# Kernel tuning notes

Hardware: AMD Instinct MI355X
Metric: run time of the kernel (lower is better)

The kernel has to match this reference:

```python
import jax, jax.numpy as jnp
import numpy as np

B, T, D = 8, 1, 4096          # batch, fresh tokens (single-token decode), d_model
H, HD, KV = 32, 128, 512      # n_heads, head_dim, mla_kv_lrank
PAST = 8191                   # cached compressed-KV length
SCALE = HD ** -0.5


def setup_inputs() -> dict:
    key = jax.random.key(0)
    ks = jax.random.split(key, 6)
    return {
        "x": jax.random.normal(ks[0], (B, T, D), dtype=jnp.float32),
        "past_c": jax.random.normal(ks[1], (B, PAST, KV), dtype=jnp.float32),
        # absorbed q*k_up projection: [H, D, KV]
        "absorbed_qk": jax.random.normal(ks[2], (H, D, KV), dtype=jnp.float32) * 0.02,
        # _compress_kv: Linear(D -> KV)
        "w_compress": jax.random.normal(ks[3], (D, KV), dtype=jnp.float32) * 0.02,
        # v_up: Linear(KV -> H*HD)
        "w_v": jax.random.normal(ks[4], (KV, H * HD), dtype=jnp.float32) * 0.02,
        # out_proj: Linear(H*HD -> D)
        "w_o": jax.random.normal(ks[5], (H * HD, D), dtype=jnp.float32) * 0.02,
    }


def reference(x, past_c, absorbed_qk, w_compress, w_v, w_o):
    b, t, d = x.shape
    # compress fresh tokens and extend the compressed KV cache
    c = x @ w_compress                                 # [B, T, KV]
    c_full = jnp.concatenate([past_c, c], axis=1)      # [B, total, KV]
    total = c_full.shape[1]

    # absorbed query projection: Q_abs = x @ absorbed_qk per head
    q_abs = jnp.einsum('btd,hdk->bhtk', x, absorbed_qk)        # [B, H, T, KV]
    # attention scores directly against compressed cache
    scores = jnp.einsum('bhtk,bsk->bhts', q_abs, c_full) * SCALE  # [B, H, T, total]

    # causal mask: query t (absolute pos total-T+t) sees kv pos p iff p <= total-T+t
    q_pos = jnp.arange(t)[:, None] + (total - t)       # [T, 1]
    kv_pos = jnp.arange(total)[None, :]                # [1, total]
    causal = q_pos >= kv_pos                           # [T, total]
    scores = jnp.where(causal[None, None], scores, -jnp.inf)
    attn = jax.nn.softmax(scores, axis=-1)             # [B, H, T, total]

    # up-project V from compressed cache
    v = (c_full @ w_v).reshape(b, total, H, HD)        # [B, total, H, HD]
    out = jnp.einsum('bhts,bshd->bthd', attn, v).reshape(b, t, H * HD)
    return out @ w_o                                   # [B, T, D]
```

## Files before the change

kernel.cpp:

```cpp
#include <hip/hip_runtime.h>
#include <stdint.h>

#define B_ 8
#define D_ 4096
#define H_ 32
#define HD_ 128
#define KV_ 512
#define PAST_ 8191
#define SCALE_ 0.08838834764831845f

#define OFF_QABS 0u
#define OFF_CNEW 131072u
#define OFF_ML   135168u
#define OFF_CTXP 167936u
#define OFF_CTX  8556544u
#define OFF_CTX2 8687616u

typedef float f32x4 __attribute__((ext_vector_type(4)));
typedef float f32x2 __attribute__((ext_vector_type(2)));
typedef short s16x8 __attribute__((ext_vector_type(8)));
typedef short s16x4 __attribute__((ext_vector_type(4)));

__device__ __forceinline__ unsigned short f2bf(float f) {
    unsigned u = __float_as_uint(f);
    u = (u + 0x7FFFu + ((u >> 16) & 1u)) >> 16;
    return (unsigned short)u;
}
__device__ __forceinline__ float bf2f(unsigned short s) {
    return __uint_as_float(((unsigned)s) << 16);
}

__global__ __launch_bounds__(256) void k_qabs(const float* __restrict__ x,
                                              const float* __restrict__ aqk,
                                              const float* __restrict__ wc,
                                              float* __restrict__ ws) {
    const int h = blockIdx.x;
    const int dc = blockIdx.y;
    const int t = threadIdx.x;
    alignas(16) __shared__ float x_lds[B_][512];
    for (int i = t; i < B_ * 512; i += 256) {
        const int b = i >> 9, dd = i & 511;
        x_lds[b][dd] = x[b * D_ + dc * 512 + dd];
    }
    __syncthreads();
    const float* A = (h < H_) ? (aqk + (size_t)h * D_ * KV_) : wc;
    A += (size_t)(dc * 512) * KV_ + 2 * t;

    float acc[B_][2] = {};
    for (int dd = 0; dd < 512; dd += 4) {
        f32x2 a[4];
#pragma unroll
        for (int i = 0; i < 4; ++i)
            a[i] = *(const f32x2*)(A + (size_t)(dd + i) * KV_);
#pragma unroll
        for (int b = 0; b < B_; ++b) {
            const f32x4 xv = *(const f32x4*)&x_lds[b][dd];
            acc[b][0] += xv[0] * a[0][0] + xv[1] * a[1][0] + xv[2] * a[2][0] + xv[3] * a[3][0];
            acc[b][1] += xv[0] * a[0][1] + xv[1] * a[1][1] + xv[2] * a[2][1] + xv[3] * a[3][1];
        }
    }
#pragma unroll
    for (int b = 0; b < B_; ++b) {
        float* dst = (h < H_) ? (ws + OFF_QABS + (size_t)(b * H_ + h) * KV_ + 2 * t)
                              : (ws + OFF_CNEW + (size_t)b * KV_ + 2 * t);
        atomicAdd(dst, acc[b][0]);
        atomicAdd(dst + 1, acc[b][1]);
    }
}

__global__ __launch_bounds__(256, 2) void k_attn(const float* __restrict__ past_c,
                                                 float* __restrict__ ws) {
    const int bx = blockIdx.x;
    const int b = bx >> 6, sc = bx & 63;
    const int t = threadIdx.x;
    const int w = t >> 6, lane = t & 63, quad = lane >> 4, ln = lane & 15;
    const int ni = w & 1, kh = w >> 1;

    alignas(16) __shared__ unsigned short ch[16 * 520];
    alignas(16) __shared__ unsigned short cl[16 * 520];
    alignas(16) __shared__ unsigned short cT[512 * 20];
    alignas(16) __shared__ float Sp[2 * 16 * 33];
    alignas(16) __shared__ unsigned short P[32 * 20];
    __shared__ float alpha[32];

    s16x8 qh[8], ql[8];
    {
        const float* qp = ws + OFF_QABS + (size_t)(b * H_ + ni * 16 + ln) * KV_ + kh * 256 + quad * 8;
#pragma unroll
        for (int st = 0; st < 8; ++st) {
            const f32x4 v0 = *(const f32x4*)(qp + st * 32);
            const f32x4 v1 = *(const f32x4*)(qp + st * 32 + 4);
#pragma unroll
            for (int i = 0; i < 8; ++i) {
                const float xv = ((i < 4) ? v0[i] : v1[i - 4]) * SCALE_;
                const unsigned short hi = f2bf(xv);
                qh[st][i] = (short)hi;
                ql[st][i] = (short)f2bf(xv - bf2f(hi));
            }
        }
    }

    f32x4 cacc[16];
#pragma unroll
    for (int i = 0; i < 16; ++i) cacc[i] = (f32x4){0.f, 0.f, 0.f, 0.f};
    float m_run = -1e30f, l_run = 0.f;

    for (int sub = 0; sub < 8; ++sub) {
        const int s0 = sc * 128 + sub * 16;
        {
            const int r = t >> 4, cb = (t & 15) * 32;
            const int sg = s0 + r;
            const float* src = (sg == PAST_) ? (ws + OFF_CNEW + (size_t)b * KV_)
                                             : (past_c + ((size_t)b * PAST_ + sg) * KV_);
#pragma unroll
            for (int i = 0; i < 8; ++i) {
                const int k = cb + i * 4;
                const f32x4 v = *(const f32x4*)(src + k);
                s16x4 hi4, lo4;
#pragma unroll
                for (int e = 0; e < 4; ++e) {
                    const unsigned short hh = f2bf(v[e]);
                    hi4[e] = (short)hh;
                    lo4[e] = (short)f2bf(v[e] - bf2f(hh));
                    cT[(k + e) * 20 + r] = hh;
                }
                *(s16x4*)&ch[r * 520 + k] = hi4;
                *(s16x4*)&cl[r * 520 + k] = lo4;
            }
        }
        __syncthreads();
        {
            f32x4 sacc = {0.f, 0.f, 0.f, 0.f};
#pragma unroll
            for (int st = 0; st < 8; ++st) {
                const int ko = kh * 256 + st * 32 + quad * 8;
                const s16x8 ah = *(const s16x8*)&ch[ln * 520 + ko];
                const s16x8 al = *(const s16x8*)&cl[ln * 520 + ko];
                sacc = __builtin_amdgcn_mfma_f32_16x16x32_bf16(ah, qh[st], sacc, 0, 0, 0);
                sacc = __builtin_amdgcn_mfma_f32_16x16x32_bf16(ah, ql[st], sacc, 0, 0, 0);
                sacc = __builtin_amdgcn_mfma_f32_16x16x32_bf16(al, qh[st], sacc, 0, 0, 0);
            }
#pragma unroll
            for (int r = 0; r < 4; ++r)
                Sp[kh * 528 + (quad * 4 + r) * 33 + ni * 16 + ln] = sacc[r];
        }
        __syncthreads();
        if (t < 32) {
            const int h = t;
            float sv[16];
            float msub = -1e30f;
#pragma unroll
            for (int s = 0; s < 16; ++s) {
                sv[s] = Sp[s * 33 + h] + Sp[528 + s * 33 + h];
                msub = fmaxf(msub, sv[s]);
            }
            const float m_new = fmaxf(m_run, msub);
            const float al_ = __expf(m_run - m_new);
            float lsum = 0.f;
#pragma unroll
            for (int s = 0; s < 16; s += 2) {
                const float p0 = __expf(sv[s] - m_new);
                const float p1 = __expf(sv[s + 1] - m_new);
                lsum += p0 + p1;
                const unsigned pk = (unsigned)f2bf(p0) | ((unsigned)f2bf(p1) << 16);
                *(unsigned*)&P[h * 20 + s] = pk;
            }
            l_run = l_run * al_ + lsum;
            m_run = m_new;
            alpha[h] = al_;
        }
        __syncthreads();
        {
            const float av = alpha[ni * 16 + ln];
            const s16x4 bp = *(const s16x4*)&P[(ni * 16 + ln) * 20 + quad * 4];
#pragma unroll
            for (int ti = 0; ti < 16; ++ti) {
                const int krow = (kh * 16 + ti) * 16 + ln;
                const s16x4 ac = *(const s16x4*)&cT[krow * 20 + quad * 4];
                f32x4 cc = cacc[ti];
                cc[0] *= av; cc[1] *= av; cc[2] *= av; cc[3] *= av;
                cacc[ti] = __builtin_amdgcn_mfma_f32_16x16x16bf16_1k(ac, bp, cc, 0, 0, 0);
            }
        }
        __syncthreads();
    }
    {
        float* cp = ws + OFF_CTXP + ((size_t)(b * 64 + sc) * H_ + (ni * 16 + ln)) * KV_;
#pragma unroll
        for (int ti = 0; ti < 16; ++ti) {
            const int k0 = (kh * 16 + ti) * 16 + quad * 4;
            *(f32x4*)(cp + k0) = cacc[ti];
        }
    }
    if (t < 32) {
        float* mp = ws + OFF_ML + (size_t)(b * 64 + sc) * 64;
        mp[t] = m_run;
        mp[32 + t] = l_run;
    }
}

__global__ __launch_bounds__(256) void k_comb(float* __restrict__ ws) {
    const int b = blockIdx.x >> 5, h = blockIdx.x & 31;
    const int t = threadIdx.x;
    __shared__ float ml[64], ll[64];
    if (t < 64) {
        const float* mp = ws + OFF_ML + (size_t)(b * 64 + t) * 64;
        ml[t] = mp[h];
        ll[t] = mp[32 + h];
    }
    __syncthreads();
    float M = -1e30f;
    for (int sc = 0; sc < 64; ++sc) M = fmaxf(M, ml[sc]);
    float L = 0.f;
    for (int sc = 0; sc < 64; ++sc) L += ll[sc] * __expf(ml[sc] - M);
    const float invL = 1.f / L;
    float a0 = 0.f, a1 = 0.f;
    for (int sc = 0; sc < 64; ++sc) {
        const float wgt = __expf(ml[sc] - M) * invL;
        const float* cp = ws + OFF_CTXP + ((size_t)(b * 64 + sc) * H_ + h) * KV_;
        a0 += wgt * cp[t];
        a1 += wgt * cp[256 + t];
    }
    float* o = ws + OFF_CTX + (size_t)(b * H_ + h) * KV_;
    o[t] = a0;
    o[256 + t] = a1;
}

__global__ __launch_bounds__(256) void k_vup(const float* __restrict__ wv, float* __restrict__ ws) {
    const int b = blockIdx.x >> 5, h = blockIdx.x & 31;
    const int t = threadIdx.x;
    alignas(16) __shared__ float cx[512];
    __shared__ float red[256];
    cx[t] = ws[OFF_CTX + (size_t)(b * H_ + h) * KV_ + t];
    cx[t + 256] = ws[OFF_CTX + (size_t)(b * H_ + h) * KV_ + t + 256];
    __syncthreads();
    const int khalf = t >> 7, hd = t & 127;
    const float* wp = wv + (size_t)(khalf * 256) * (H_ * HD_) + h * HD_ + hd;
    float acc = 0.f;
#pragma unroll 8
    for (int k = 0; k < 256; ++k)
        acc += cx[khalf * 256 + k] * wp[(size_t)k * (H_ * HD_)];
    red[t] = acc;
    __syncthreads();
    if (t < 128)
        ws[OFF_CTX2 + (size_t)b * (H_ * HD_) + h * HD_ + t] = red[t] + red[128 + t];
}

__global__ __launch_bounds__(256) void k_out(const float* __restrict__ wo,
                                             const float* __restrict__ ws,
                                             float* __restrict__ out) {
    const int dc = blockIdx.x, jc = blockIdx.y;
    const int t = threadIdx.x;
    alignas(16) __shared__ float c2[B_][256];
#pragma unroll
    for (int i = 0; i < 8; ++i) {
        const int e = t + i * 256;
        const int bb = e >> 8, jj = e & 255;
        c2[bb][jj] = ws[OFF_CTX2 + (size_t)bb * D_ + jc * 256 + jj];
    }
    __syncthreads();
    const int d = dc * 256 + t;
    float acc[B_] = {};
    for (int j = 0; j < 256; j += 4) {
        const float w0 = wo[(size_t)(jc * 256 + j) * D_ + d];
        const float w1 = wo[(size_t)(jc * 256 + j + 1) * D_ + d];
        const float w2 = wo[(size_t)(jc * 256 + j + 2) * D_ + d];
        const float w3 = wo[(size_t)(jc * 256 + j + 3) * D_ + d];
#pragma unroll
        for (int b = 0; b < B_; ++b) {
            const f32x4 cv = *(const f32x4*)&c2[b][j];
            acc[b] += cv[0] * w0 + cv[1] * w1 + cv[2] * w2 + cv[3] * w3;
        }
    }
#pragma unroll
    for (int b = 0; b < B_; ++b)
        atomicAdd(&out[b * D_ + d], acc[b]);
}

extern "C" void kernel_launch(void* const* d_in, const int* in_sizes, int n_in,
                              void* d_out, int out_size, void* d_ws, size_t ws_size,
                              hipStream_t stream) {
    const float* x      = (const float*)d_in[0];
    const float* past_c = (const float*)d_in[1];
    const float* aqk    = (const float*)d_in[2];
    const float* wc     = (const float*)d_in[3];
    const float* wv     = (const float*)d_in[4];
    const float* wo     = (const float*)d_in[5];
    float* out = (float*)d_out;
    float* ws  = (float*)d_ws;

    hipMemsetAsync(ws, 0, (size_t)OFF_ML * sizeof(float), stream);
    hipMemsetAsync(d_out, 0, (size_t)out_size * sizeof(float), stream);

    k_qabs<<<dim3(33, 8), 256, 0, stream>>>(x, aqk, wc, ws);
    k_attn<<<dim3(512), 256, 0, stream>>>(past_c, ws);
    k_comb<<<dim3(256), 256, 0, stream>>>(ws);
    k_vup<<<dim3(256), 256, 0, stream>>>(wv, ws);
    k_out<<<dim3(16, 16), 256, 0, stream>>>(wo, ws, out);
}
```

Baseline: 595.0 us.

## Split q-abs reduction, swizzle cT LDS, fuse combine with V-up, widen loads

The q-abs projection now uses 16 D-chunks with 128 threads and float4 weight loads. It writes partial sums to the workspace, and a new reduction kernel adds them up, replacing float atomics and the workspace memset. In the attention kernel the transposed-cache LDS writes are XOR-swizzled to cut bank conflicts, and the global load pattern is changed. The softmax-combine and V-up kernels are fused into one with vectorized loads, which removes a launch and a workspace round trip. The output projection loop is unrolled by 8. The cost is an extra launch for the reduction and more workspace traffic for the partial sums.

```diff
diff --git a/kernel.cpp b/kernel.cpp
--- a/kernel.cpp
+++ b/kernel.cpp
@@ -9,12 +9,13 @@
 #define PAST_ 8191
 #define SCALE_ 0.08838834764831845f
 
-#define OFF_QABS 0u
-#define OFF_CNEW 131072u
-#define OFF_ML   135168u
-#define OFF_CTXP 167936u
-#define OFF_CTX  8556544u
-#define OFF_CTX2 8687616u
+#define OFF_QP   0u
+#define OFF_CP   2097152u
+#define OFF_QABS 2162688u
+#define OFF_CNEW 2293760u
+#define OFF_ML   2297856u
+#define OFF_CTXP 2330624u
+#define OFF_CTX2 10719232u
 
 typedef float f32x4 __attribute__((ext_vector_type(4)));
 typedef float f32x2 __attribute__((ext_vector_type(2)));
@@ -30,41 +31,69 @@
     return __uint_as_float(((unsigned)s) << 16);
 }
 
-__global__ __launch_bounds__(256) void k_qabs(const float* __restrict__ x,
+__global__ __launch_bounds__(128) void k_qabs(const float* __restrict__ x,
                                               const float* __restrict__ aqk,
                                               const float* __restrict__ wc,
                                               float* __restrict__ ws) {
     const int h = blockIdx.x;
     const int dc = blockIdx.y;
     const int t = threadIdx.x;
-    alignas(16) __shared__ float x_lds[B_][512];
-    for (int i = t; i < B_ * 512; i += 256) {
-        const int b = i >> 9, dd = i & 511;
-        x_lds[b][dd] = x[b * D_ + dc * 512 + dd];
+    alignas(16) __shared__ float x_lds[B_][256];
+    for (int i = t; i < 512; i += 128) {
+        const int b = i >> 6, g = i & 63;
+        *(f32x4*)&x_lds[b][g * 4] = *(const f32x4*)(x + (size_t)b * D_ + dc * 256 + g * 4);
     }
     __syncthreads();
     const float* A = (h < H_) ? (aqk + (size_t)h * D_ * KV_) : wc;
-    A += (size_t)(dc * 512) * KV_ + 2 * t;
-
-    float acc[B_][2] = {};
-    for (int dd = 0; dd < 512; dd += 4) {
-        f32x2 a[4];
-#pragma unroll
-        for (int i = 0; i < 4; ++i)
-            a[i] = *(const f32x2*)(A + (size_t)(dd + i) * KV_);
+    A += ((size_t)dc * 256) * KV_ + t * 4;
+
+    f32x4 acc[B_];
+#pragma unroll
+    for (int b = 0; b < B_; ++b) acc[b] = (f32x4){0.f, 0.f, 0.f, 0.f};
+
+#pragma unroll 2
+    for (int dd = 0; dd < 256; dd += 4) {
+        const f32x4 a0 = *(const f32x4*)(A + (size_t)(dd + 0) * KV_);
+        const f32x4 a1 = *(const f32x4*)(A + (size_t)(dd + 1) * KV_);
+        const f32x4 a2 = *(const f32x4*)(A + (size_t)(dd + 2) * KV_);
+        const f32x4 a3 = *(const f32x4*)(A + (size_t)(dd + 3) * KV_);
 #pragma unroll
         for (int b = 0; b < B_; ++b) {
-            const f32x4 xv = *(const f32x4*)&x_lds[b][dd];
-            acc[b][0] += xv[0] * a[0][0] + xv[1] * a[1][0] + xv[2] * a[2][0] + xv[3] * a[3][0];
-            acc[b][1] += xv[0] * a[0][1] + xv[1] * a[1][1] + xv[2] * a[2][1] + xv[3] * a[3][1];
+            const f32x4 xq = *(const f32x4*)&x_lds[b][dd];
+            acc[b] += xq.x * a0 + xq.y * a1 + xq.z * a2 + xq.w * a3;
         }
     }
 #pragma unroll
     for (int b = 0; b < B_; ++b) {
-        float* dst = (h < H_) ? (ws + OFF_QABS + (size_t)(b * H_ + h) * KV_ + 2 * t)
-                              : (ws + OFF_CNEW + (size_t)b * KV_ + 2 * t);
-        atomicAdd(dst, acc[b][0]);
-        atomicAdd(dst + 1, acc[b][1]);
+        float* dst = (h < H_)
+            ? (ws + OFF_QP + (size_t)dc * 131072u + (size_t)(b * H_ + h) * KV_ + t * 4)
+            : (ws + OFF_CP + (size_t)dc * 4096u + (size_t)b * KV_ + t * 4);
+        *(f32x4*)dst = acc[b];
+    }
+}
+
+__global__ __launch_bounds__(256) void k_qred(float* __restrict__ ws) {
+    const int bx = blockIdx.x;
+    const int t = threadIdx.x;
+    if (bx < 256) {
+        const int b = bx >> 5, h = bx & 31;
+        const size_t row = (size_t)(b * H_ + h) * KV_;
+        f32x2 s = {0.f, 0.f};
+#pragma unroll
+        for (int p = 0; p < 16; ++p) {
+            const f32x2 v = *(const f32x2*)(ws + OFF_QP + (size_t)p * 131072u + row + 2 * t);
+            s[0] += v[0]; s[1] += v[1];
+        }
+        *(f32x2*)(ws + OFF_QABS + row + 2 * t) = s;
+    } else {
+        const int b = bx - 256;
+        f32x2 s = {0.f, 0.f};
+#pragma unroll
+        for (int p = 0; p < 16; ++p) {
+            const f32x2 v = *(const f32x2*)(ws + OFF_CP + (size_t)p * 4096u + (size_t)b * KV_ + 2 * t);
+            s[0] += v[0]; s[1] += v[1];
+        }
+        *(f32x2*)(ws + OFF_CNEW + (size_t)b * KV_ + 2 * t) = s;
     }
 }
 
@@ -108,13 +137,13 @@
     for (int sub = 0; sub < 8; ++sub) {
         const int s0 = sc * 128 + sub * 16;
         {
-            const int r = t >> 4, cb = (t & 15) * 32;
+            const int r = t >> 4, m = t & 15;
             const int sg = s0 + r;
             const float* src = (sg == PAST_) ? (ws + OFF_CNEW + (size_t)b * KV_)
                                              : (past_c + ((size_t)b * PAST_ + sg) * KV_);
 #pragma unroll
             for (int i = 0; i < 8; ++i) {
-                const int k = cb + i * 4;
+                const int k = m * 4 + i * 64;
                 const f32x4 v = *(const f32x4*)(src + k);
                 s16x4 hi4, lo4;
 #pragma unroll
@@ -122,7 +151,8 @@
                     const unsigned short hh = f2bf(v[e]);
                     hi4[e] = (short)hh;
                     lo4[e] = (short)f2bf(v[e] - bf2f(hh));
-                    cT[(k + e) * 20 + r] = hh;
+                    const int kk = k + e;
+                    cT[kk * 20 + (r ^ ((((kk) >> 4) & 3) << 2))] = hh;
                 }
                 *(s16x4*)&ch[r * 520 + k] = hi4;
                 *(s16x4*)&cl[r * 520 + k] = lo4;
@@ -176,7 +206,8 @@
 #pragma unroll
             for (int ti = 0; ti < 16; ++ti) {
                 const int krow = (kh * 16 + ti) * 16 + ln;
-                const s16x4 ac = *(const s16x4*)&cT[krow * 20 + quad * 4];
+                const int sg2 = (quad ^ ((krow >> 4) & 3)) << 2;
+                const s16x4 ac = *(const s16x4*)&cT[krow * 20 + sg2];
                 f32x4 cc = cacc[ti];
                 cc[0] *= av; cc[1] *= av; cc[2] *= av; cc[3] *= av;
                 cacc[ti] = __builtin_amdgcn_mfma_f32_16x16x16bf16_1k(ac, bp, cc, 0, 0, 0);
@@ -199,10 +230,13 @@
     }
 }
 
-__global__ __launch_bounds__(256) void k_comb(float* __restrict__ ws) {
+__global__ __launch_bounds__(256) void k_cv(const float* __restrict__ wv,
+                                            float* __restrict__ ws) {
     const int b = blockIdx.x >> 5, h = blockIdx.x & 31;
     const int t = threadIdx.x;
-    __shared__ float ml[64], ll[64];
+    __shared__ float ml[64], ll[64], wgt[64];
+    alignas(16) __shared__ float cx[512];
+    alignas(16) __shared__ float red[8][128];
     if (t < 64) {
         const float* mp = ws + OFF_ML + (size_t)(b * 64 + t) * 64;
         ml[t] = mp[h];
@@ -210,40 +244,36 @@
     }
     __syncthreads();
     float M = -1e30f;
-    for (int sc = 0; sc < 64; ++sc) M = fmaxf(M, ml[sc]);
+    for (int s = 0; s < 64; ++s) M = fmaxf(M, ml[s]);
+    if (t < 64) wgt[t] = __expf(ml[t] - M);
+    __syncthreads();
     float L = 0.f;
-    for (int sc = 0; sc < 64; ++sc) L += ll[sc] * __expf(ml[sc] - M);
+    for (int s = 0; s < 64; ++s) L += ll[s] * wgt[s];
     const float invL = 1.f / L;
-    float a0 = 0.f, a1 = 0.f;
-    for (int sc = 0; sc < 64; ++sc) {
-        const float wgt = __expf(ml[sc] - M) * invL;
-        const float* cp = ws + OFF_CTXP + ((size_t)(b * 64 + sc) * H_ + h) * KV_;
-        a0 += wgt * cp[t];
-        a1 += wgt * cp[256 + t];
-    }
-    float* o = ws + OFF_CTX + (size_t)(b * H_ + h) * KV_;
-    o[t] = a0;
-    o[256 + t] = a1;
-}
-
-__global__ __launch_bounds__(256) void k_vup(const float* __restrict__ wv, float* __restrict__ ws) {
-    const int b = blockIdx.x >> 5, h = blockIdx.x & 31;
-    const int t = threadIdx.x;
-    alignas(16) __shared__ float cx[512];
-    __shared__ float red[256];
-    cx[t] = ws[OFF_CTX + (size_t)(b * H_ + h) * KV_ + t];
-    cx[t + 256] = ws[OFF_CTX + (size_t)(b * H_ + h) * KV_ + t + 256];
-    __syncthreads();
-    const int khalf = t >> 7, hd = t & 127;
-    const float* wp = wv + (size_t)(khalf * 256) * (H_ * HD_) + h * HD_ + hd;
-    float acc = 0.f;
-#pragma unroll 8
-    for (int k = 0; k < 256; ++k)
-        acc += cx[khalf * 256 + k] * wp[(size_t)k * (H_ * HD_)];
-    red[t] = acc;
-    __syncthreads();
-    if (t < 128)
-        ws[OFF_CTX2 + (size_t)b * (H_ * HD_) + h * HD_ + t] = red[t] + red[128 + t];
+    f32x2 acc = {0.f, 0.f};
+    for (int s = 0; s < 64; ++s) {
+        const float f = wgt[s];
+        const f32x2 v = *(const f32x2*)(ws + OFF_CTXP + ((size_t)(b * 64 + s) * H_ + h) * KV_ + 2 * t);
+        acc[0] += f * v[0];
+        acc[1] += f * v[1];
+    }
+    *(f32x2*)&cx[2 * t] = (f32x2){acc[0] * invL, acc[1] * invL};
+    __syncthreads();
+    const int r = t >> 5, c = (t & 31) * 4;
+    f32x4 a4 = {0.f, 0.f, 0.f, 0.f};
+    for (int kb = 0; kb < 64; ++kb) {
+        const int k = kb * 8 + r;
+        const f32x4 w4 = *(const f32x4*)(wv + (size_t)k * (H_ * HD_) + h * HD_ + c);
+        a4 += cx[k] * w4;
+    }
+    *(f32x4*)&red[r][c] = a4;
+    __syncthreads();
+    if (t < 128) {
+        float s = 0.f;
+#pragma unroll
+        for (int rr = 0; rr < 8; ++rr) s += red[rr][t];
+        ws[OFF_CTX2 + (size_t)b * D_ + h * HD_ + t] = s;
+    }
 }
 
 __global__ __launch_bounds__(256) void k_out(const float* __restrict__ wo,
@@ -261,15 +291,17 @@
     __syncthreads();
     const int d = dc * 256 + t;
     float acc[B_] = {};
-    for (int j = 0; j < 256; j += 4) {
-        const float w0 = wo[(size_t)(jc * 256 + j) * D_ + d];
-        const float w1 = wo[(size_t)(jc * 256 + j + 1) * D_ + d];
-        const float w2 = wo[(size_t)(jc * 256 + j + 2) * D_ + d];
-        const float w3 = wo[(size_t)(jc * 256 + j + 3) * D_ + d];
+    for (int j = 0; j < 256; j += 8) {
+        float wreg[8];
+#pragma unroll
+        for (int u = 0; u < 8; ++u)
+            wreg[u] = wo[(size_t)(jc * 256 + j + u) * D_ + d];
 #pragma unroll
         for (int b = 0; b < B_; ++b) {
-            const f32x4 cv = *(const f32x4*)&c2[b][j];
-            acc[b] += cv[0] * w0 + cv[1] * w1 + cv[2] * w2 + cv[3] * w3;
+            const f32x4 c0 = *(const f32x4*)&c2[b][j];
+            const f32x4 c1 = *(const f32x4*)&c2[b][j + 4];
+            acc[b] += c0[0] * wreg[0] + c0[1] * wreg[1] + c0[2] * wreg[2] + c0[3] * wreg[3]
+                    + c1[0] * wreg[4] + c1[1] * wreg[5] + c1[2] * wreg[6] + c1[3] * wreg[7];
         }
     }
 #pragma unroll
@@ -289,12 +321,11 @@
     float* out = (float*)d_out;
     float* ws  = (float*)d_ws;
 
-    hipMemsetAsync(ws, 0, (size_t)OFF_ML * sizeof(float), stream);
     hipMemsetAsync(d_out, 0, (size_t)out_size * sizeof(float), stream);
 
-    k_qabs<<<dim3(33, 8), 256, 0, stream>>>(x, aqk, wc, ws);
+    k_qabs<<<dim3(33, 16), 128, 0, stream>>>(x, aqk, wc, ws);
+    k_qred<<<dim3(264), 256, 0, stream>>>(ws);
     k_attn<<<dim3(512), 256, 0, stream>>>(past_c, ws);
-    k_comb<<<dim3(256), 256, 0, stream>>>(ws);
-    k_vup<<<dim3(256), 256, 0, stream>>>(wv, ws);
+    k_cv<<<dim3(256), 256, 0, stream>>>(wv, ws);
     k_out<<<dim3(16, 16), 256, 0, stream>>>(wo, ws, out);
 }
```

New measurement: 550.0 us. -7.6%, faster.
